# Kernel tuning notes

Hardware: AMD Instinct MI355X
Metric: run time of the kernel (lower is better)

The kernel has to match this reference:

```python
import jax, jax.numpy as jnp
import numpy as np

L = 3          # num_layers
EPS = 1e-5     # BatchNorm eps


def _gmn_forward(feats_1, feats_2, edge_index_1, edge_index_2, N1, N2,
                 Wn, bn, Wm, bm, Wp, bp, gamma, beta, Wa, ba, Wg, bg, Wf, bf):
    N = N1 + N2
    x = jnp.concatenate([feats_1, feats_2], axis=0)                       # [N, F]
    edge_index = jnp.concatenate([edge_index_1, edge_index_2 + N1], axis=1)
    src, dst = edge_index[0], edge_index[1]                               # source_to_target flow
    batch = jnp.concatenate([jnp.zeros((N1,), jnp.int32), jnp.ones((N2,), jnp.int32)])
    for l in range(L):
        h = x @ Wn[l] + bn[l]                                             # lin_node
        # message(x_i=h[dst], x_j=h[src]) = lin_message(cat[x_i, x_j])
        m = jnp.concatenate([h[dst], h[src]], axis=1) @ Wm[l] + bm[l]     # [E, D]
        aggr = jax.ops.segment_sum(m, dst, num_segments=N)                # scatter-add to targets
        # batch_block_pair_attention on ORIGINAL (pre-lin_node) features
        gx, gy = x[:N1], x[N1:]
        s = gx @ gy.T                                                     # [N1, N2] similarities
        att_x = jax.nn.softmax(s, axis=1) @ gy                            # attn for graph-1 nodes
        att_y = jax.nn.softmax(s, axis=0).T @ gx                          # attn for graph-2 nodes
        cross = jnp.concatenate([att_x, att_y], axis=0)                   # [N, F]
        att_in = x - cross                                                # attention_input
        out = jnp.concatenate([aggr, att_in], axis=1) @ Wp[l] + bp[l]     # lin_passing
        mu = out.mean(axis=0)
        var = ((out - mu) ** 2).mean(axis=0)                              # BatchNorm (train, biased var)
        x = (out - mu) * jax.lax.rsqrt(var + EPS) * gamma[l] + beta[l]
    # GraphAggregator
    states = x @ Wa + ba
    gates = jax.nn.softmax(x @ Wg + bg, axis=1)                           # softmax over feature dim (as in source)
    g = states * gates
    sums = jax.ops.segment_sum(g, batch, num_segments=2)                  # scatter_mean
    counts = jnp.array([N1, N2], jnp.float32)[:, None]
    emb = (sums / counts) @ Wf + bf                                       # [2, D]
    return emb


def setup_inputs() -> dict:
    key = jax.random.key(0)
    ks = jax.random.split(key, 12)
    N1 = N2 = 6144
    E = 196608
    F = 128
    D = 128
    sc = lambda fan: fan ** -0.5
    rn = lambda k, sh, s: jax.random.normal(k, sh, dtype=jnp.float32) * s
    return {
        "feats_1": rn(ks[0], (N1, F), 1.0),
        "edge_index_1": jax.random.randint(ks[1], (2, E), 0, N1),
        "feats_2": rn(ks[2], (N2, F), 1.0),
        "edge_index_2": jax.random.randint(ks[3], (2, E), 0, N2),
        "sizes_1": N1,
        "sizes_2": N2,
        "Wn": rn(ks[4], (L, F, D), sc(F)),
        "bn": jnp.zeros((L, D), jnp.float32),
        "Wm": rn(ks[5], (L, 2 * D, D), sc(2 * D)),
        "bm": jnp.zeros((L, D), jnp.float32),
        "Wp": rn(ks[6], (L, D + F, D), sc(D + F)),
        "bp": jnp.zeros((L, D), jnp.float32),
        "gamma": jnp.ones((L, D), jnp.float32),
        "beta": jnp.zeros((L, D), jnp.float32),
        "Wa": rn(ks[7], (D, D), sc(D)),
        "ba": jnp.zeros((D,), jnp.float32),
        "Wg": rn(ks[8], (D, D), sc(D)),
        "bg": jnp.zeros((D,), jnp.float32),
        "Wf": rn(ks[9], (D, D), sc(D)),
        "bf": jnp.zeros((D,), jnp.float32),
    }


def reference(feats_1, edge_index_1, feats_2, edge_index_2, sizes_1, sizes_2,
              Wn, bn, Wm, bm, Wp, bp, gamma, beta, Wa, ba, Wg, bg, Wf, bf):
    emb = _gmn_forward(feats_1, feats_2, edge_index_1, edge_index_2,
                       int(sizes_1), int(sizes_2),
                       Wn, bn, Wm, bm, Wp, bp, gamma, beta, Wa, ba, Wg, bg, Wf, bf)
    emb_1 = emb[0:1]
    emb_2 = emb[1:2]
    return emb_1, emb_2
```

## Files before the change

kernel.cpp:

```cpp
#include <hip/hip_runtime.h>
#include <hip/hip_bf16.h>

#define D 128
#define KVS 8
typedef unsigned short u16;
typedef unsigned int u32;
typedef __attribute__((ext_vector_type(8))) short short8;
typedef __attribute__((ext_vector_type(16))) float f32x16;
typedef __attribute__((ext_vector_type(4))) u32 u32x4;

__device__ __forceinline__ u16 f2bf(float f){
  u32 u = __builtin_bit_cast(u32, f);
  u32 r = (u + 0x7FFFu + ((u >> 16) & 1u)) >> 16;
  return (u16)r;
}
__device__ __forceinline__ float bf2f(u16 u){
  union { u32 i; float f; } v; v.i = ((u32)u) << 16; return v.f;
}

__global__ void k_count(const int* __restrict__ ei1, const int* __restrict__ ei2,
                        int E1, int E2, int N1, int* __restrict__ cnt){
  int i = blockIdx.x*blockDim.x + threadIdx.x;
  int Et = E1 + E2;
  for (; i < Et; i += gridDim.x*blockDim.x){
    int dst = (i < E1) ? ei1[E1 + i] : (ei2[E2 + (i - E1)] + N1);
    atomicAdd(&cnt[dst], 1);
  }
}

__global__ void k_scan(const int* __restrict__ cnt, int* __restrict__ ptr,
                       int* __restrict__ cursor, float* __restrict__ degf, int N){
  __shared__ int part[256];
  int t = threadIdx.x;
  int per = (N + 255) >> 8;
  int lo = t*per, hi = min(N, lo+per);
  int s = 0;
  for (int j=lo;j<hi;j++) s += cnt[j];
  part[t] = s; __syncthreads();
  if (t==0){ int acc=0; for (int j=0;j<256;j++){ int v=part[j]; part[j]=acc; acc+=v; } }
  __syncthreads();
  int acc = part[t];
  for (int j=lo;j<hi;j++){ ptr[j]=acc; cursor[j]=acc; degf[j]=(float)cnt[j]; acc += cnt[j]; }
}

__global__ void k_fill(const int* __restrict__ ei1, const int* __restrict__ ei2,
                       int E1, int E2, int N1, int* __restrict__ cursor, int* __restrict__ srclist){
  int i = blockIdx.x*blockDim.x + threadIdx.x;
  int Et = E1 + E2;
  for (; i < Et; i += gridDim.x*blockDim.x){
    int src, dst;
    if (i < E1){ src = ei1[i]; dst = ei1[E1+i]; }
    else { int j = i - E1; src = ei2[j] + N1; dst = ei2[E2+j] + N1; }
    int p = atomicAdd(&cursor[dst], 1);
    srclist[p] = src;
  }
}

__global__ __launch_bounds__(256) void k_wcvt(const float* __restrict__ Wp, const float* __restrict__ Wa,
                                              const float* __restrict__ Wg, u16* __restrict__ wgt){
  __shared__ u16 tile[128][136];
  int m = blockIdx.x;
  const float* src; u16* dst;
  if (m < 6){ int l = m % 3, half = m / 3; src = Wp + (size_t)l*32768 + half*16384; dst = wgt + (size_t)(half*3 + l)*16384; }
  else if (m == 6){ src = Wa; dst = wgt + (size_t)6*16384; }
  else { src = Wg; dst = wgt + (size_t)7*16384; }
  int t = threadIdx.x;
  int n = t & 127, rh = t >> 7;
  for (int r0=0; r0<128; r0+=2){
    int r = r0 + rh;
    tile[n][r] = f2bf(src[r*128 + n]);
  }
  __syncthreads();
  int row = t >> 1, ch = t & 1;
  #pragma unroll
  for (int i=0;i<4;i++){
    int k0 = ch*64 + i*16;
    short8 a = *(const short8*)&tile[row][k0];
    short8 b = *(const short8*)&tile[row][k0+8];
    *(short8*)&dst[row*128 + k0] = a;
    *(short8*)&dst[row*128 + k0 + 8] = b;
  }
}

__global__ __launch_bounds__(256) void k_wfuse(const float* __restrict__ Wn, const float* __restrict__ Wm,
                                               const float* __restrict__ bn, const float* __restrict__ bm,
                                               u16* __restrict__ wfu, float* __restrict__ fbias){
  int blk = blockIdx.x;
  int l = blk % 3, which = blk / 3;
  const float* A  = Wn + (size_t)l*16384;
  const float* Bm = Wm + (size_t)l*32768 + (which==0 ? 16384 : 0);
  u16* dst  = wfu  + (size_t)(which==0 ? l : 3+l)*16384;
  float* fb = fbias + (size_t)(which==0 ? l : 3+l)*128;
  int t = threadIdx.x;
  int c0 = (t & 31) * 4;
  int r0 = (t >> 5) * 16;
  float acc[16][4];
  #pragma unroll
  for (int i=0;i<16;i++){ acc[i][0]=0.f; acc[i][1]=0.f; acc[i][2]=0.f; acc[i][3]=0.f; }
  for (int k=0;k<128;k++){
    float4 b4 = *(const float4*)&Bm[k*128 + c0];
    #pragma unroll
    for (int i=0;i<16;i++){
      float a = A[(r0+i)*128 + k];
      acc[i][0] += a*b4.x; acc[i][1] += a*b4.y; acc[i][2] += a*b4.z; acc[i][3] += a*b4.w;
    }
  }
  #pragma unroll
  for (int i=0;i<16;i++)
    #pragma unroll
    for (int j=0;j<4;j++)
      dst[(size_t)(c0+j)*128 + (r0+i)] = f2bf(acc[i][j]);
  if (t < 128){
    float s = 0.f;
    for (int k=0;k<128;k++) s += bn[l*128+k]*Bm[k*128+t];
    if (which) s += bm[l*128+t];
    fb[t] = s;
  }
}

__global__ __launch_bounds__(256) void k_cvt0(const float* __restrict__ src1, const float* __restrict__ src2,
                                              int N1, float* __restrict__ x, u16* __restrict__ xb,
                                              u16* __restrict__ xbT, int N){
  __shared__ u16 tile[128][136];
  int nb = blockIdx.x * 128;
  int t = threadIdx.x;
  int n = t >> 1;
  int ch = t & 1;
  int row = nb + n;
  const float* srow = (row < N1) ? &src1[(size_t)row*D] : &src2[(size_t)(row-N1)*D];
  #pragma unroll
  for (int i=0;i<16;i++){
    int dd = ch*64 + i*4;
    float4 v = *(const float4*)&srow[dd];
    *(float4*)&x[(size_t)row*D + dd] = v;
    u16 b0 = f2bf(v.x), b1 = f2bf(v.y), b2 = f2bf(v.z), b3 = f2bf(v.w);
    ushort4 uv; uv.x=b0; uv.y=b1; uv.z=b2; uv.w=b3;
    *(ushort4*)&xb[(size_t)row*D + dd] = uv;
    tile[dd+0][n]=b0; tile[dd+1][n]=b1; tile[dd+2][n]=b2; tile[dd+3][n]=b3;
  }
  __syncthreads();
  int d = t & 127, hf = t >> 7;
  #pragma unroll
  for (int i=0;i<8;i++){
    short8 v = *(const short8*)&tile[d][hf*64 + i*8];
    *(short8*)&xbT[(size_t)d*N + nb + hf*64 + i*8] = v;
  }
}

__global__ __launch_bounds__(256) void k_gemm(
    const u16* __restrict__ A, const u16* __restrict__ W1T,
    const u16* __restrict__ B, const u16* __restrict__ W2T,
    const float* __restrict__ bias, const float* __restrict__ bias2,
    const float* __restrict__ rs, const float* __restrict__ addin,
    float* __restrict__ of, float* __restrict__ of2,
    u16* __restrict__ ob, float* __restrict__ csums, int N)
{
  __shared__ __align__(16) u16 Wsw[2][16384];
  const int t = threadIdx.x;
  const int w4 = t >> 6;
  const int lane = t & 63;
  const int l31 = lane & 31;
  const int hi = lane >> 5;
  const int rb = blockIdx.x * 32;

  #pragma unroll
  for (int i=0;i<8;i++){
    int slot = i*256 + t;
    int row = slot >> 4, g = slot & 15;
    short8 v = *(const short8*)(W1T + row*128 + g*8);
    *(short8*)((char*)&Wsw[0][0] + row*256 + ((g ^ (row&7))*16)) = v;
  }
  if (B){
    #pragma unroll
    for (int i=0;i<8;i++){
      int slot = i*256 + t;
      int row = slot >> 4, g = slot & 15;
      short8 v = *(const short8*)(W2T + row*128 + g*8);
      *(short8*)((char*)&Wsw[1][0] + row*256 + ((g ^ (row&7))*16)) = v;
    }
  }
  short8 af[8], bfr[8];
  #pragma unroll
  for (int g=0; g<8; g++)
    af[g] = *(const short8*)(A + (size_t)(rb + l31)*D + (2*g + hi)*8);
  if (B){
    #pragma unroll
    for (int g=0; g<8; g++)
      bfr[g] = *(const short8*)(B + (size_t)(rb + l31)*D + (2*g + hi)*8);
  }
  __syncthreads();

  f32x16 acc1, acc2;
  #pragma unroll
  for (int i=0;i<16;i++){ acc1[i]=0.f; acc2[i]=0.f; }
  const int wrow = w4*32 + l31;
  #pragma unroll
  for (int s=0;s<8;s++){
    int gr = 2*s + hi;
    short8 wf = *(const short8*)((const char*)&Wsw[0][0] + wrow*256 + ((gr ^ (wrow&7))*16));
    acc1 = __builtin_amdgcn_mfma_f32_32x32x16_bf16(af[s], wf, acc1, 0,0,0);
  }
  if (B){
    #pragma unroll
    for (int s=0;s<8;s++){
      int gr = 2*s + hi;
      short8 wf = *(const short8*)((const char*)&Wsw[1][0] + wrow*256 + ((gr ^ (wrow&7))*16));
      acc2 = __builtin_amdgcn_mfma_f32_32x32x16_bf16(bfr[s], wf, acc2, 0,0,0);
    }
  }
  const int col = wrow;
  float bv = bias ? bias[col] : 0.0f;
  float bv2 = bias2 ? bias2[col] : 0.0f;
  float ssum = 0.f, sq = 0.f;
  #pragma unroll
  for (int r=0;r<16;r++){
    int rr = (r&3) + 8*(r>>2) + 4*hi;
    size_t grow = (size_t)(rb + rr);
    float v = acc1[r] + bv;
    if (rs) v *= rs[grow];
    if (addin) v += addin[grow*D + col];
    if (B && !of2) v += acc2[r];
    if (of) of[grow*D + col] = v;
    if (ob) ob[grow*D + col] = f2bf(v);
    if (of2) of2[grow*D + col] = acc2[r] + bv2;
    ssum += v; sq += v*v;
  }
  if (csums){
    ssum += __shfl_xor(ssum, 32, 64);
    sq   += __shfl_xor(sq, 32, 64);
    if (hi == 0){
      atomicAdd(&csums[col], ssum);
      atomicAdd(&csums[128+col], sq);
    }
  }
}

__global__ __launch_bounds__(256) void k_gather(const u16* __restrict__ hb, const int* __restrict__ ptr,
                          const int* __restrict__ cnt, const int* __restrict__ srclist,
                          float* __restrict__ Sg, int N){
  int f = threadIdx.x & 127, sub = threadIdx.x >> 7;
  int v = blockIdx.x*2 + sub;
  if (v >= N) return;
  int b = ptr[v], n = cnt[v];
  float a0=0.f, a1=0.f, a2=0.f, a3=0.f;
  int j=0;
  for (; j+3<n; j+=4){
    int s0=srclist[b+j], s1=srclist[b+j+1], s2=srclist[b+j+2], s3=srclist[b+j+3];
    a0 += bf2f(hb[(size_t)s0*D + f]);
    a1 += bf2f(hb[(size_t)s1*D + f]);
    a2 += bf2f(hb[(size_t)s2*D + f]);
    a3 += bf2f(hb[(size_t)s3*D + f]);
  }
  for (; j<n; j++) a0 += bf2f(hb[(size_t)srclist[b+j]*D + f]);
  Sg[(size_t)v*D + f] = (a0+a1)+(a2+a3);
}

__global__ __launch_bounds__(256, 2) void k_flash_mfma(
    const u16* __restrict__ xb, const u16* __restrict__ xbT,
    int N1, int N2, int Ntot,
    u16* __restrict__ Opartb, float* __restrict__ MLpart)
{
  __shared__ __align__(16) u16 Kbuf[2][4096];
  __shared__ __align__(16) u16 Vbuf[2][4096];

  const float L2E = 1.44269504f;
  const int t = threadIdx.x;
  const int w = t >> 6;
  const int lane = t & 63;
  const int l31 = lane & 31;
  const int hi = lane >> 5;

  const int qb = blockIdx.x / KVS;
  const int sp = blockIdx.x % KVS;
  const int qbase = qb * 128;
  const int qs = qbase + w*32;
  const bool isY = qbase >= N1;
  const int kv0 = isY ? 0 : N1;
  const int kvlen = isY ? N1 : N2;
  const int Lk = kvlen / KVS;
  const int kstart = kv0 + sp*Lk;
  const int ntiles = Lk >> 5;

  short8 qf[8];
  #pragma unroll
  for (int c = 0; c < 8; ++c)
    qf[c] = *(const short8*)(xb + (size_t)(qs + l31)*D + c*16 + hi*8);

  const int kr = t >> 3;
  const int kg = (t & 7) * 2;
  const int vd = t >> 1;
  const int vj = (t & 1) * 2;
  const int kw0 = kr*256 + ((kg     ^ (kr & 7))*16);
  const int kw1 = kr*256 + (((kg+1) ^ (kr & 7))*16);
  const int vw0 = vd*64  + (((vj     ^ vd) & 3)*16);
  const int vw1 = vd*64  + ((((vj+1) ^ vd) & 3)*16);

  f32x16 O[4];
  #pragma unroll
  for (int mt=0; mt<4; ++mt)
    #pragma unroll
    for (int i=0;i<16;i++) O[mt][i] = 0.f;
  float m_run = -3.0e38f, l_run = 0.0f;

  {
    int kb = kstart;
    short8 a0 = *(const short8*)(xb  + (size_t)(kb+kr)*D + kg*8);
    short8 a1 = *(const short8*)(xb  + (size_t)(kb+kr)*D + (kg+1)*8);
    short8 v0 = *(const short8*)(xbT + (size_t)vd*Ntot + kb + vj*8);
    short8 v1 = *(const short8*)(xbT + (size_t)vd*Ntot + kb + (vj+1)*8);
    *(short8*)((char*)&Kbuf[0][0] + kw0) = a0;
    *(short8*)((char*)&Kbuf[0][0] + kw1) = a1;
    *(short8*)((char*)&Vbuf[0][0] + vw0) = v0;
    *(short8*)((char*)&Vbuf[0][0] + vw1) = v1;
  }
  __syncthreads();

  for (int tt = 0; tt < ntiles; ++tt){
    const int cur = tt & 1;
    const int nxt = cur ^ 1;
    short8 a0, a1, v0, v1;
    const bool more = (tt+1 < ntiles);
    if (more){
      int kb = kstart + (tt+1)*32;
      a0 = *(const short8*)(xb  + (size_t)(kb+kr)*D + kg*8);
      a1 = *(const short8*)(xb  + (size_t)(kb+kr)*D + (kg+1)*8);
      v0 = *(const short8*)(xbT + (size_t)vd*Ntot + kb + vj*8);
      v1 = *(const short8*)(xbT + (size_t)vd*Ntot + kb + (vj+1)*8);
    }

    const char* Klds = (const char*)&Kbuf[cur][0];
    const char* Vlds = (const char*)&Vbuf[cur][0];

    f32x16 sa, sb;
    #pragma unroll
    for (int i=0;i<16;i++){ sa[i]=0.f; sb[i]=0.f; }
    #pragma unroll
    for (int c = 0; c < 8; c += 2){
      int gr0 = 2*c + hi;
      short8 ka = *(const short8*)(Klds + l31*256 + ((gr0 ^ (l31&7))*16));
      sa = __builtin_amdgcn_mfma_f32_32x32x16_bf16(ka, qf[c], sa, 0,0,0);
      int gr1 = 2*(c+1) + hi;
      short8 kbf = *(const short8*)(Klds + l31*256 + ((gr1 ^ (l31&7))*16));
      sb = __builtin_amdgcn_mfma_f32_32x32x16_bf16(kbf, qf[c+1], sb, 0,0,0);
    }
    f32x16 s;
    #pragma unroll
    for (int i=0;i<16;i++) s[i] = sa[i] + sb[i];

    float tm = s[0];
    #pragma unroll
    for (int i=1;i<16;i++) tm = fmaxf(tm, s[i]);
    tm = fmaxf(tm, __shfl_xor(tm, 32, 64));
    float tm2 = tm * L2E;
    if (__any(tm2 > m_run + 11.544f)){
      float mnew = fmaxf(m_run, tm2);
      float alpha = exp2f(m_run - mnew);
      l_run *= alpha;
      m_run = mnew;
      #pragma unroll
      for (int i=0;i<16;i++){ O[0][i]*=alpha; O[1][i]*=alpha; O[2][i]*=alpha; O[3][i]*=alpha; }
    }
    float rsum = 0.f;
    #pragma unroll
    for (int i=0;i<16;i++){ float p = exp2f(fmaf(s[i], L2E, -m_run)); s[i]=p; rsum += p; }
    rsum += __shfl_xor(rsum, 32, 64);
    l_run += rsum;

    u32 pk[8];
    #pragma unroll
    for (int i=0;i<8;i++){
      u32 r;
      asm("v_cvt_pk_bf16_f32 %0, %1, %2" : "=v"(r) : "v"(s[2*i]), "v"(s[2*i+1]));
      pk[i] = r;
    }

    #pragma unroll
    for (int ks=0; ks<2; ++ks){
      u32 send0 = hi ? pk[(2*ks)*2+0] : pk[(2*ks+1)*2+0];
      u32 send1 = hi ? pk[(2*ks)*2+1] : pk[(2*ks+1)*2+1];
      u32 xv0 = (u32)__shfl_xor((int)send0, 32, 64);
      u32 xv1 = (u32)__shfl_xor((int)send1, 32, 64);
      u32 own0 = hi ? pk[(2*ks+1)*2+0] : pk[(2*ks)*2+0];
      u32 own1 = hi ? pk[(2*ks+1)*2+1] : pk[(2*ks)*2+1];
      u32x4 bv;
      bv.x = hi ? xv0 : own0;
      bv.y = hi ? xv1 : own1;
      bv.z = hi ? own0 : xv0;
      bv.w = hi ? own1 : xv1;
      short8 pf = __builtin_bit_cast(short8, bv);
      #pragma unroll
      for (int mt=0; mt<4; ++mt){
        int dd = mt*32 + l31;
        int j = 2*ks + hi;
        short8 vf = *(const short8*)(Vlds + dd*64 + (((j ^ dd) & 3)*16));
        O[mt] = __builtin_amdgcn_mfma_f32_32x32x16_bf16(vf, pf, O[mt], 0,0,0);
      }
    }

    if (more){
      *(short8*)((char*)&Kbuf[nxt][0] + kw0) = a0;
      *(short8*)((char*)&Kbuf[nxt][0] + kw1) = a1;
      *(short8*)((char*)&Vbuf[nxt][0] + vw0) = v0;
      *(short8*)((char*)&Vbuf[nxt][0] + vw1) = v1;
    }
    __syncthreads();
  }

  const int strip = qs >> 5;
  u16* Od = Opartb + ((size_t)strip*KVS + sp)*4096;
  #pragma unroll
  for (int mt=0; mt<4; ++mt){
    #pragma unroll
    for (int r=0;r<16;r++){
      int dd = mt*32 + (r&3) + 8*(r>>2) + 4*hi;
      Od[dd*32 + l31] = f2bf(O[mt][r]);
    }
  }
  if (lane < 32){
    float* mlp = MLpart + ((size_t)strip*KVS + sp)*64;
    mlp[l31*2+0] = m_run;
    mlp[l31*2+1] = l_run;
  }
}

__global__ __launch_bounds__(256) void k_fcomb_hm2(
    const u16* __restrict__ Opartb, const float* __restrict__ MLpart,
    const float* __restrict__ x, u16* __restrict__ attinb,
    const u16* __restrict__ xb, const u16* __restrict__ W1T, const float* __restrict__ fb2,
    u16* __restrict__ hm2b, int nstrips, int N)
{
  __shared__ __align__(16) char smem[32768];
  const int t = threadIdx.x;
  if ((int)blockIdx.x < nstrips){
    const int strip = blockIdx.x;
    float (*cw)[32] = (float(*)[32])smem;
    float (*Tld)[33] = (float(*)[33])(smem + 1024);
    if (t < 32){
      const float* mlp = MLpart + (size_t)strip*KVS*64;
      float mv[KVS], lv[KVS];
      float M = -3.0e38f;
      #pragma unroll
      for (int s2=0;s2<KVS;s2++){ mv[s2]=mlp[s2*64+t*2]; lv[s2]=mlp[s2*64+t*2+1]; M = fmaxf(M, mv[s2]); }
      float L = 0.f;
      #pragma unroll
      for (int s2=0;s2<KVS;s2++){ float wv=exp2f(mv[s2]-M); cw[s2][t]=wv; L += wv*lv[s2]; }
      float inv = 1.0f / L;
      #pragma unroll
      for (int s2=0;s2<KVS;s2++) cw[s2][t] *= inv;
    }
    __syncthreads();
    {
      const int d = t >> 1, q0 = (t & 1) * 16;
      const u16* Ob = Opartb + (size_t)strip*KVS*4096;
      float acc[16];
      #pragma unroll
      for (int j=0;j<16;j++) acc[j]=0.f;
      #pragma unroll
      for (int s2=0; s2<KVS; ++s2){
        const u16* row = Ob + s2*4096 + d*32 + q0;
        short8 v8a = *(const short8*)row;
        short8 v8b = *(const short8*)(row + 8);
        #pragma unroll
        for (int j=0;j<8;j++){
          acc[j]   += cw[s2][q0+j]  *bf2f((u16)v8a[j]);
          acc[8+j] += cw[s2][q0+8+j]*bf2f((u16)v8b[j]);
        }
      }
      #pragma unroll
      for (int j=0;j<16;j++) Tld[d][q0+j] = acc[j];
    }
    __syncthreads();
    {
      const int q = t >> 3, c0 = (t & 7) * 16;
      const size_t row = (size_t)(strip*32 + q)*D;
      #pragma unroll
      for (int i=0;i<16;i+=4){
        float4 xr = *(const float4*)&x[row + c0 + i];
        ushort4 o;
        o.x = f2bf(xr.x - Tld[c0+i+0][q]);
        o.y = f2bf(xr.y - Tld[c0+i+1][q]);
        o.z = f2bf(xr.z - Tld[c0+i+2][q]);
        o.w = f2bf(xr.w - Tld[c0+i+3][q]);
        *(ushort4*)&attinb[row + c0 + i] = o;
      }
    }
  } else {
    u16* Wsw = (u16*)smem;
    const int w4 = t >> 6;
    const int lane = t & 63;
    const int l31 = lane & 31;
    const int hi = lane >> 5;
    const int rb = ((int)blockIdx.x - nstrips) * 32;
    #pragma unroll
    for (int i=0;i<8;i++){
      int slot = i*256 + t;
      int row = slot >> 4, g = slot & 15;
      short8 v = *(const short8*)(W1T + row*128 + g*8);
      *(short8*)((char*)Wsw + row*256 + ((g ^ (row&7))*16)) = v;
    }
    short8 af[8];
    #pragma unroll
    for (int g=0; g<8; g++)
      af[g] = *(const short8*)(xb + (size_t)(rb + l31)*D + (2*g + hi)*8);
    __syncthreads();
    f32x16 acc1;
    #pragma unroll
    for (int i=0;i<16;i++) acc1[i]=0.f;
    const int wrow = w4*32 + l31;
    #pragma unroll
    for (int s=0;s<8;s++){
      int gr = 2*s + hi;
      short8 wf = *(const short8*)((const char*)Wsw + wrow*256 + ((gr ^ (wrow&7))*16));
      acc1 = __builtin_amdgcn_mfma_f32_32x32x16_bf16(af[s], wf, acc1, 0,0,0);
    }
    float bv = fb2[wrow];
    #pragma unroll
    for (int r=0;r<16;r++){
      int rr = (r&3) + 8*(r>>2) + 4*hi;
      hm2b[(size_t)(rb + rr)*D + wrow] = f2bf(acc1[r] + bv);
    }
  }
}

__global__ __launch_bounds__(256) void k_normcvt(const float* __restrict__ outb,
                        const float* __restrict__ sums,
                        const float* __restrict__ gamma, const float* __restrict__ beta,
                        int N, float* __restrict__ x, u16* __restrict__ xb, u16* __restrict__ xbT){
  __shared__ u16 tile[128][136];
  __shared__ float smu[128], srs[128], sg2[128], sb2[128];
  int t = threadIdx.x;
  if (t < 128){
    float mu = sums[t] / (float)N;
    float var = fmaxf(sums[128+t]/(float)N - mu*mu, 0.0f);
    smu[t]=mu; srs[t]=rsqrtf(var + 1e-5f);
    sg2[t]=gamma[t]; sb2[t]=beta[t];
  }
  __syncthreads();
  int nb = blockIdx.x * 128;
  int n = t >> 1, ch = t & 1;
  #pragma unroll
  for (int i=0;i<16;i++){
    int dd = ch*64 + i*4;
    float4 v = *(const float4*)&outb[(size_t)(nb+n)*D + dd];
    float4 y;
    y.x = (v.x - smu[dd+0])*srs[dd+0]*sg2[dd+0] + sb2[dd+0];
    y.y = (v.y - smu[dd+1])*srs[dd+1]*sg2[dd+1] + sb2[dd+1];
    y.z = (v.z - smu[dd+2])*srs[dd+2]*sg2[dd+2] + sb2[dd+2];
    y.w = (v.w - smu[dd+3])*srs[dd+3]*sg2[dd+3] + sb2[dd+3];
    *(float4*)&x[(size_t)(nb+n)*D + dd] = y;
    u16 b0=f2bf(y.x), b1=f2bf(y.y), b2=f2bf(y.z), b3=f2bf(y.w);
    ushort4 uv; uv.x=b0; uv.y=b1; uv.z=b2; uv.w=b3;
    *(ushort4*)&xb[(size_t)(nb+n)*D + dd] = uv;
    tile[dd+0][n]=b0; tile[dd+1][n]=b1; tile[dd+2][n]=b2; tile[dd+3][n]=b3;
  }
  __syncthreads();
  int d = t & 127, hf = t >> 7;
  #pragma unroll
  for (int i=0;i<8;i++){
    short8 v = *(const short8*)&tile[d][hf*64 + i*8];
    *(short8*)&xbT[(size_t)d*N + nb + hf*64 + i*8] = v;
  }
}

__global__ __launch_bounds__(256) void k_gatepool(
    const float* __restrict__ states, const float* __restrict__ glog,
    int N1, int N, float* __restrict__ gsums)
{
  __shared__ float part[256];
  part[threadIdx.x] = 0.f;
  __syncthreads();
  int wid = threadIdx.x >> 6, lane = threadIdx.x & 63;
  for (int v = blockIdx.x*4 + wid; v < N; v += gridDim.x*4){
    float a0 = glog[(size_t)v*D + lane], a1 = glog[(size_t)v*D + lane + 64];
    float mx = fmaxf(a0,a1);
    #pragma unroll
    for (int off=32; off; off>>=1) mx = fmaxf(mx, __shfl_xor(mx, off, 64));
    float e0 = __expf(a0-mx), e1 = __expf(a1-mx);
    float ss = e0+e1;
    #pragma unroll
    for (int off=32; off; off>>=1) ss += __shfl_xor(ss, off, 64);
    float inv = 1.f/ss;
    int g = (v < N1) ? 0 : 1;
    atomicAdd(&part[g*128 + lane], states[(size_t)v*D+lane]*e0*inv);
    atomicAdd(&part[g*128 + lane + 64], states[(size_t)v*D+lane+64]*e1*inv);
  }
  __syncthreads();
  atomicAdd(&gsums[threadIdx.x], part[threadIdx.x]);
}

__global__ __launch_bounds__(256) void k_emb(
    const float* __restrict__ gsums, const float* __restrict__ Wf,
    const float* __restrict__ bf_, int N1, int N2, float* __restrict__ outp)
{
  __shared__ float mean[256];
  int t = threadIdx.x;
  mean[t] = gsums[t] / ((t < 128) ? (float)N1 : (float)N2);
  __syncthreads();
  int g = t >> 7, dc = t & 127;
  float acc = bf_[dc];
  for (int k=0;k<D;k++) acc += mean[g*128 + k] * Wf[k*D + dc];
  outp[t] = acc;
}

extern "C" void kernel_launch(void* const* d_in, const int* in_sizes, int n_in,
                              void* d_out, int out_size, void* d_ws, size_t ws_size,
                              hipStream_t stream) {
  const float* feats1 = (const float*)d_in[0];
  const int*   ei1    = (const int*)d_in[1];
  const float* feats2 = (const float*)d_in[2];
  const int*   ei2    = (const int*)d_in[3];
  const float* Wn = (const float*)d_in[6];
  const float* bn = (const float*)d_in[7];
  const float* Wm = (const float*)d_in[8];
  const float* bm = (const float*)d_in[9];
  const float* Wp = (const float*)d_in[10];
  const float* bp = (const float*)d_in[11];
  const float* gamma = (const float*)d_in[12];
  const float* beta  = (const float*)d_in[13];
  const float* Wa = (const float*)d_in[14];
  const float* ba = (const float*)d_in[15];
  const float* Wg = (const float*)d_in[16];
  const float* bg = (const float*)d_in[17];
  const float* Wf = (const float*)d_in[18];
  const float* bff = (const float*)d_in[19];

  int N1 = in_sizes[0]/D, E1 = in_sizes[1]/2;
  int N2 = in_sizes[2]/D, E2 = in_sizes[3]/2;
  int N = N1+N2;
  int nstrips = N/32;

  char* w = (char*)d_ws;
  float* x    = (float*)w; w += (size_t)N*D*4;
  u16* xb     = (u16*)w;   w += (size_t)N*D*2;
  u16* xbT    = (u16*)w;   w += (size_t)N*D*2;
  u16* hm2b   = (u16*)w;   w += (size_t)N*D*2;
  u16* aggrb  = (u16*)w;   w += (size_t)N*D*2;
  u16* attinb = (u16*)w;   w += (size_t)N*D*2;
  int* cnt    = (int*)w;   w += (size_t)N*4;
  float* sums = (float*)w; w += 3*256*4;
  float* gsums= (float*)w; w += 256*4;
  int* ptr    = (int*)w;   w += (size_t)N*4;
  int* cursor = (int*)w;   w += (size_t)N*4;
  float* degf = (float*)w; w += (size_t)N*4;
  int* srclist= (int*)w;   w += (size_t)(E1+E2)*4;
  u16* wgt    = (u16*)w;   w += (size_t)8*16384*2;
  u16* wfu    = (u16*)w;   w += (size_t)6*16384*2;
  float* fbias= (float*)w; w += (size_t)6*128*4;
  u16* Opartb = (u16*)w;   w += (size_t)nstrips*KVS*4096*2;
  float* MLpart=(float*)w; w += (size_t)nstrips*KVS*64*4;
  float* Sg     = (float*)Opartb;
  float* outb   = (float*)Opartb + (size_t)N*D;
  float* states = Sg;
  float* glog   = outb;

  hipMemsetAsync(cnt, 0, (size_t)N*4 + 4*256*4, stream);
  k_count<<<1024,256,0,stream>>>(ei1, ei2, E1, E2, N1, cnt);
  k_scan<<<1,256,0,stream>>>(cnt, ptr, cursor, degf, N);
  k_fill<<<1024,256,0,stream>>>(ei1, ei2, E1, E2, N1, cursor, srclist);
  k_wcvt<<<8,256,0,stream>>>(Wp, Wa, Wg, wgt);
  k_wfuse<<<6,256,0,stream>>>(Wn, Wm, bn, bm, wfu, fbias);
  k_cvt0<<<N/128,256,0,stream>>>(feats1, feats2, N1, x, xb, xbT, N);

  for (int l=0;l<3;l++){
    const u16* fuse2T_l = wfu + (size_t)l*16384;
    const u16* fuse1T_l = wfu + (size_t)(3+l)*16384;
    const float* fb2_l  = fbias + (size_t)l*128;
    const float* fb1_l  = fbias + (size_t)(3+l)*128;
    const u16* Wp1T_l = wgt + (size_t)(0+l)*16384;
    const u16* Wp2T_l = wgt + (size_t)(3+l)*16384;
    const float* bp_l = bp + (size_t)l*D;
    float* sums_l = sums + (size_t)l*256;

    k_flash_mfma<<<(N/128)*KVS,256,0,stream>>>(xb, xbT, N1, N2, N, Opartb, MLpart);
    k_fcomb_hm2<<<nstrips + N/32,256,0,stream>>>(Opartb, MLpart, x, attinb,
                                                 xb, fuse2T_l, fb2_l, hm2b, nstrips, N);
    k_gather<<<N/2,256,0,stream>>>(hm2b, ptr, cnt, srclist, Sg, N);
    k_gemm<<<N/32,256,0,stream>>>(xb, fuse1T_l, nullptr, nullptr, fb1_l, nullptr,
                                  degf, Sg, nullptr, nullptr, aggrb, nullptr, N);
    k_gemm<<<N/32,256,0,stream>>>(aggrb, Wp1T_l, attinb, Wp2T_l, bp_l, nullptr,
                                  nullptr, nullptr, outb, nullptr, nullptr, sums_l, N);
    k_normcvt<<<N/128,256,0,stream>>>(outb, sums_l, gamma + (size_t)l*D, beta + (size_t)l*D, N, x, xb, xbT);
  }

  k_gemm<<<N/32,256,0,stream>>>(xb, wgt + (size_t)6*16384, xb, wgt + (size_t)7*16384,
                                ba, bg, nullptr, nullptr, states, glog, nullptr, nullptr, N);
  k_gatepool<<<64,256,0,stream>>>(states, glog, N1, N, gsums);
  k_emb<<<1,256,0,stream>>>(gsums, Wf, bff, N1, N2, (float*)d_out);
}
```

Measured before the change: 657.0 us.

## Double KV splits, merge prep kernels, use single MFMA accumulator chain

Raises the number of key/value splits in the flash cross-attention from 8 to 16, giving more blocks for parallelism at the cost of more partial results to combine. Merges the weight conversion, weight fusion and input conversion kernels into one launch to cut launch overhead. Replaces the two interleaved MFMA accumulators for the score tile with a single dependent chain, which saves registers but serialises the MFMAs. The combine kernel's shared-memory offset is moved to make room for the larger per-split weight table.

```diff
diff --git a/kernel.cpp b/kernel.cpp
--- a/kernel.cpp
+++ b/kernel.cpp
@@ -2,7 +2,7 @@
 #include <hip/hip_bf16.h>
 
 #define D 128
-#define KVS 8
+#define KVS 16
 typedef unsigned short u16;
 typedef unsigned int u32;
 typedef __attribute__((ext_vector_type(8))) short short8;
@@ -56,94 +56,90 @@
   }
 }
 
-__global__ __launch_bounds__(256) void k_wcvt(const float* __restrict__ Wp, const float* __restrict__ Wa,
-                                              const float* __restrict__ Wg, u16* __restrict__ wgt){
+__global__ __launch_bounds__(256) void k_prep(
+    const float* __restrict__ Wp, const float* __restrict__ Wa, const float* __restrict__ Wg,
+    const float* __restrict__ Wn, const float* __restrict__ Wm,
+    const float* __restrict__ bn, const float* __restrict__ bm,
+    const float* __restrict__ src1, const float* __restrict__ src2, int N1,
+    u16* __restrict__ wgt, u16* __restrict__ wfu, float* __restrict__ fbias,
+    float* __restrict__ x, u16* __restrict__ xb, u16* __restrict__ xbT, int N)
+{
   __shared__ u16 tile[128][136];
-  int m = blockIdx.x;
-  const float* src; u16* dst;
-  if (m < 6){ int l = m % 3, half = m / 3; src = Wp + (size_t)l*32768 + half*16384; dst = wgt + (size_t)(half*3 + l)*16384; }
-  else if (m == 6){ src = Wa; dst = wgt + (size_t)6*16384; }
-  else { src = Wg; dst = wgt + (size_t)7*16384; }
-  int t = threadIdx.x;
-  int n = t & 127, rh = t >> 7;
-  for (int r0=0; r0<128; r0+=2){
-    int r = r0 + rh;
-    tile[n][r] = f2bf(src[r*128 + n]);
-  }
-  __syncthreads();
-  int row = t >> 1, ch = t & 1;
-  #pragma unroll
-  for (int i=0;i<4;i++){
-    int k0 = ch*64 + i*16;
-    short8 a = *(const short8*)&tile[row][k0];
-    short8 b = *(const short8*)&tile[row][k0+8];
-    *(short8*)&dst[row*128 + k0] = a;
-    *(short8*)&dst[row*128 + k0 + 8] = b;
-  }
-}
-
-__global__ __launch_bounds__(256) void k_wfuse(const float* __restrict__ Wn, const float* __restrict__ Wm,
-                                               const float* __restrict__ bn, const float* __restrict__ bm,
-                                               u16* __restrict__ wfu, float* __restrict__ fbias){
-  int blk = blockIdx.x;
-  int l = blk % 3, which = blk / 3;
-  const float* A  = Wn + (size_t)l*16384;
-  const float* Bm = Wm + (size_t)l*32768 + (which==0 ? 16384 : 0);
-  u16* dst  = wfu  + (size_t)(which==0 ? l : 3+l)*16384;
-  float* fb = fbias + (size_t)(which==0 ? l : 3+l)*128;
-  int t = threadIdx.x;
-  int c0 = (t & 31) * 4;
-  int r0 = (t >> 5) * 16;
-  float acc[16][4];
-  #pragma unroll
-  for (int i=0;i<16;i++){ acc[i][0]=0.f; acc[i][1]=0.f; acc[i][2]=0.f; acc[i][3]=0.f; }
-  for (int k=0;k<128;k++){
-    float4 b4 = *(const float4*)&Bm[k*128 + c0];
+  const int m = blockIdx.x;
+  const int t = threadIdx.x;
+  if (m < 8){
+    const float* src; u16* dst;
+    if (m < 6){ int l = m % 3, half = m / 3; src = Wp + (size_t)l*32768 + half*16384; dst = wgt + (size_t)(half*3 + l)*16384; }
+    else if (m == 6){ src = Wa; dst = wgt + (size_t)6*16384; }
+    else { src = Wg; dst = wgt + (size_t)7*16384; }
+    int n = t & 127, rh = t >> 7;
+    for (int r0=0; r0<128; r0+=2){
+      int r = r0 + rh;
+      tile[n][r] = f2bf(src[r*128 + n]);
+    }
+    __syncthreads();
+    int row = t >> 1, ch = t & 1;
+    #pragma unroll
+    for (int i=0;i<4;i++){
+      int k0 = ch*64 + i*16;
+      short8 a = *(const short8*)&tile[row][k0];
+      short8 b = *(const short8*)&tile[row][k0+8];
+      *(short8*)&dst[row*128 + k0] = a;
+      *(short8*)&dst[row*128 + k0 + 8] = b;
+    }
+  } else if (m < 14){
+    int blk = m - 8;
+    int l = blk % 3, which = blk / 3;
+    const float* A  = Wn + (size_t)l*16384;
+    const float* Bm = Wm + (size_t)l*32768 + (which==0 ? 16384 : 0);
+    u16* dst  = wfu  + (size_t)(which==0 ? l : 3+l)*16384;
+    float* fb = fbias + (size_t)(which==0 ? l : 3+l)*128;
+    int c0 = (t & 31) * 4;
+    int r0 = (t >> 5) * 16;
+    float acc[16][4];
+    #pragma unroll
+    for (int i=0;i<16;i++){ acc[i][0]=0.f; acc[i][1]=0.f; acc[i][2]=0.f; acc[i][3]=0.f; }
+    for (int k=0;k<128;k++){
+      float4 b4 = *(const float4*)&Bm[k*128 + c0];
+      #pragma unroll
+      for (int i=0;i<16;i++){
+        float a = A[(r0+i)*128 + k];
+        acc[i][0] += a*b4.x; acc[i][1] += a*b4.y; acc[i][2] += a*b4.z; acc[i][3] += a*b4.w;
+      }
+    }
+    #pragma unroll
+    for (int i=0;i<16;i++)
+      #pragma unroll
+      for (int j=0;j<4;j++)
+        dst[(size_t)(c0+j)*128 + (r0+i)] = f2bf(acc[i][j]);
+    if (t < 128){
+      float s = 0.f;
+      for (int k=0;k<128;k++) s += bn[l*128+k]*Bm[k*128+t];
+      if (which) s += bm[l*128+t];
+      fb[t] = s;
+    }
+  } else {
+    int nb = (m - 14) * 128;
+    int n = t >> 1, ch = t & 1;
+    int row = nb + n;
+    const float* srow = (row < N1) ? &src1[(size_t)row*D] : &src2[(size_t)(row-N1)*D];
     #pragma unroll
     for (int i=0;i<16;i++){
-      float a = A[(r0+i)*128 + k];
-      acc[i][0] += a*b4.x; acc[i][1] += a*b4.y; acc[i][2] += a*b4.z; acc[i][3] += a*b4.w;
-    }
-  }
-  #pragma unroll
-  for (int i=0;i<16;i++)
-    #pragma unroll
-    for (int j=0;j<4;j++)
-      dst[(size_t)(c0+j)*128 + (r0+i)] = f2bf(acc[i][j]);
-  if (t < 128){
-    float s = 0.f;
-    for (int k=0;k<128;k++) s += bn[l*128+k]*Bm[k*128+t];
-    if (which) s += bm[l*128+t];
-    fb[t] = s;
-  }
-}
-
-__global__ __launch_bounds__(256) void k_cvt0(const float* __restrict__ src1, const float* __restrict__ src2,
-                                              int N1, float* __restrict__ x, u16* __restrict__ xb,
-                                              u16* __restrict__ xbT, int N){
-  __shared__ u16 tile[128][136];
-  int nb = blockIdx.x * 128;
-  int t = threadIdx.x;
-  int n = t >> 1;
-  int ch = t & 1;
-  int row = nb + n;
-  const float* srow = (row < N1) ? &src1[(size_t)row*D] : &src2[(size_t)(row-N1)*D];
-  #pragma unroll
-  for (int i=0;i<16;i++){
-    int dd = ch*64 + i*4;
-    float4 v = *(const float4*)&srow[dd];
-    *(float4*)&x[(size_t)row*D + dd] = v;
-    u16 b0 = f2bf(v.x), b1 = f2bf(v.y), b2 = f2bf(v.z), b3 = f2bf(v.w);
-    ushort4 uv; uv.x=b0; uv.y=b1; uv.z=b2; uv.w=b3;
-    *(ushort4*)&xb[(size_t)row*D + dd] = uv;
-    tile[dd+0][n]=b0; tile[dd+1][n]=b1; tile[dd+2][n]=b2; tile[dd+3][n]=b3;
-  }
-  __syncthreads();
-  int d = t & 127, hf = t >> 7;
-  #pragma unroll
-  for (int i=0;i<8;i++){
-    short8 v = *(const short8*)&tile[d][hf*64 + i*8];
-    *(short8*)&xbT[(size_t)d*N + nb + hf*64 + i*8] = v;
+      int dd = ch*64 + i*4;
+      float4 v = *(const float4*)&srow[dd];
+      *(float4*)&x[(size_t)row*D + dd] = v;
+      u16 b0 = f2bf(v.x), b1 = f2bf(v.y), b2 = f2bf(v.z), b3 = f2bf(v.w);
+      ushort4 uv; uv.x=b0; uv.y=b1; uv.z=b2; uv.w=b3;
+      *(ushort4*)&xb[(size_t)row*D + dd] = uv;
+      tile[dd+0][n]=b0; tile[dd+1][n]=b1; tile[dd+2][n]=b2; tile[dd+3][n]=b3;
+    }
+    __syncthreads();
+    int d = t & 127, hf = t >> 7;
+    #pragma unroll
+    for (int i=0;i<8;i++){
+      short8 v = *(const short8*)&tile[d][hf*64 + i*8];
+      *(short8*)&xbT[(size_t)d*N + nb + hf*64 + i*8] = v;
+    }
   }
 }
 
@@ -331,21 +327,15 @@
     const char* Klds = (const char*)&Kbuf[cur][0];
     const char* Vlds = (const char*)&Vbuf[cur][0];
 
-    f32x16 sa, sb;
-    #pragma unroll
-    for (int i=0;i<16;i++){ sa[i]=0.f; sb[i]=0.f; }
-    #pragma unroll
-    for (int c = 0; c < 8; c += 2){
-      int gr0 = 2*c + hi;
-      short8 ka = *(const short8*)(Klds + l31*256 + ((gr0 ^ (l31&7))*16));
-      sa = __builtin_amdgcn_mfma_f32_32x32x16_bf16(ka, qf[c], sa, 0,0,0);
-      int gr1 = 2*(c+1) + hi;
-      short8 kbf = *(const short8*)(Klds + l31*256 + ((gr1 ^ (l31&7))*16));
-      sb = __builtin_amdgcn_mfma_f32_32x32x16_bf16(kbf, qf[c+1], sb, 0,0,0);
-    }
     f32x16 s;
     #pragma unroll
-    for (int i=0;i<16;i++) s[i] = sa[i] + sb[i];
+    for (int i=0;i<16;i++) s[i]=0.f;
+    #pragma unroll
+    for (int c = 0; c < 8; ++c){
+      int gr = 2*c + hi;
+      short8 ka = *(const short8*)(Klds + l31*256 + ((gr ^ (l31&7))*16));
+      s = __builtin_amdgcn_mfma_f32_32x32x16_bf16(ka, qf[c], s, 0,0,0);
+    }
 
     float tm = s[0];
     #pragma unroll
@@ -434,7 +424,7 @@
   if ((int)blockIdx.x < nstrips){
     const int strip = blockIdx.x;
     float (*cw)[32] = (float(*)[32])smem;
-    float (*Tld)[33] = (float(*)[33])(smem + 1024);
+    float (*Tld)[33] = (float(*)[33])(smem + 2048);
     if (t < 32){
       const float* mlp = MLpart + (size_t)strip*KVS*64;
       float mv[KVS], lv[KVS];
@@ -657,9 +647,8 @@
   k_count<<<1024,256,0,stream>>>(ei1, ei2, E1, E2, N1, cnt);
   k_scan<<<1,256,0,stream>>>(cnt, ptr, cursor, degf, N);
   k_fill<<<1024,256,0,stream>>>(ei1, ei2, E1, E2, N1, cursor, srclist);
-  k_wcvt<<<8,256,0,stream>>>(Wp, Wa, Wg, wgt);
-  k_wfuse<<<6,256,0,stream>>>(Wn, Wm, bn, bm, wfu, fbias);
-  k_cvt0<<<N/128,256,0,stream>>>(feats1, feats2, N1, x, xb, xbT, N);
+  k_prep<<<14 + N/128,256,0,stream>>>(Wp, Wa, Wg, Wn, Wm, bn, bm,
+                                      feats1, feats2, N1, wgt, wfu, fbias, x, xb, xbT, N);
 
   for (int l=0;l<3;l++){
     const u16* fuse2T_l = wfu + (size_t)l*16384;
```

Result: faster. 634.6 us (-3.4%).
